# Kernel tuning notes

Hardware: AMD Instinct MI355X
Metric: run time of the kernel (lower is better)

Reference implementation:

```python
import jax, jax.numpy as jnp
from jax import lax
import numpy as np

B, D, P = 4096, 256, 512  # batch, encoded_space_dim (=d_prototypes), n_prototypes
BN_EPS = 1e-5  # torch BatchNorm eval with running_mean=0, running_var=1


def _conv(x, w, stride, pad):
    # x: NCHW, w: OIHW
    return lax.conv_general_dilated(x, w, (stride, stride), [(pad, pad), (pad, pad)],
                                    dimension_numbers=('NCHW', 'OIHW', 'NCHW'))


def _conv_t(x, w, stride, pad, out_pad):
    # torch ConvTranspose2d; w in torch layout [Cin, Cout, kh, kw]
    k = w.shape[2]
    wf = jnp.flip(w, (2, 3)).transpose(1, 0, 2, 3)  # -> OIHW, flipped
    lo = k - 1 - pad
    hi = k - 1 - pad + out_pad
    return lax.conv_general_dilated(x, wf, (1, 1), [(lo, hi), (lo, hi)],
                                    lhs_dilation=(stride, stride),
                                    dimension_numbers=('NCHW', 'OIHW', 'NCHW'))


def _bn(x, g, b):
    # eval-mode BatchNorm2d with running_mean=0, running_var=1
    s = g / jnp.sqrt(1.0 + BN_EPS)
    return x * s[None, :, None, None] + b[None, :, None, None]


def _bias(x, b):
    return x + b[None, :, None, None]


def setup_inputs() -> dict:
    key = jax.random.key(0)
    ks = jax.random.split(key, 32)
    n = jax.random.normal
    inp = {
        'x': jax.random.uniform(ks[0], (B, 1, 28, 28), jnp.float32),
        # encoder
        'w1': n(ks[1], (8, 1, 3, 3), jnp.float32) * 0.1, 'b1': jnp.zeros((8,), jnp.float32),
        'w2': n(ks[2], (16, 8, 3, 3), jnp.float32) * 0.1, 'b2': jnp.zeros((16,), jnp.float32),
        'g2': jnp.ones((16,), jnp.float32), 'bt2': jnp.zeros((16,), jnp.float32),
        'w3': n(ks[3], (D, 16, 3, 3), jnp.float32) * 0.1, 'b3': jnp.zeros((D,), jnp.float32),
        # prototypes (torch.rand init)
        'protolayer': jax.random.uniform(ks[4], (P, D, 1, 1), jnp.float32),
        # up layer (ConvTranspose2d(D, D, 5), torch layout [Cin,Cout,kh,kw])
        'wup': n(ks[5], (D, D, 5, 5), jnp.float32) * 0.02, 'bup': jnp.zeros((D,), jnp.float32),
        'gup': jnp.ones((D,), jnp.float32), 'btup': jnp.zeros((D,), jnp.float32),
        # decoder
        'wd1': n(ks[6], (D, 16, 3, 3), jnp.float32) * 0.05, 'bd1': jnp.zeros((16,), jnp.float32),
        'gd1': jnp.ones((16,), jnp.float32), 'btd1': jnp.zeros((16,), jnp.float32),
        'wd2': n(ks[7], (16, 8, 3, 3), jnp.float32) * 0.1, 'bd2': jnp.zeros((8,), jnp.float32),
        'gd2': jnp.ones((8,), jnp.float32), 'btd2': jnp.zeros((8,), jnp.float32),
        'wd3': n(ks[8], (8, 1, 3, 3), jnp.float32) * 0.1, 'bd3': jnp.zeros((1,), jnp.float32),
    }
    return inp


def reference(x, w1, b1, w2, b2, g2, bt2, w3, b3, protolayer,
              wup, bup, gup, btup,
              wd1, bd1, gd1, btd1, wd2, bd2, gd2, btd2, wd3, bd3):
    # ---- encoder: 28 -> 14 -> 7 -> 5 ----
    h = jax.nn.relu(_bias(_conv(x, w1, 2, 1), b1))
    h = jax.nn.relu(_bn(_bias(_conv(h, w2, 2, 1), b2), g2, bt2))
    h = jax.nn.relu(_bias(_conv(h, w3, 1, 0), b3))  # [B, D, 5, 5]

    # ---- l2 'convolution' with 1x1 prototypes ----
    p = protolayer[:, :, 0, 0]                                  # [P, D]
    x2_patch_sum = jnp.sum(h * h, axis=1)                       # ones-conv, 1x1 kernel -> channel sum [B,5,5]
    xp = jnp.einsum('bdhw,pd->bphw', h, p)                      # [B, P, 5, 5]
    p2 = jnp.sum(p * p, axis=1)                                 # [P]
    distances = jax.nn.relu(x2_patch_sum[:, None] - 2.0 * xp + p2[None, :, None, None])

    # min-pool over full spatial extent
    min_distances = jnp.min(distances, axis=(2, 3))             # [B, P]
    prototype_activations = -min_distances                      # 'linear' distance_2_similarity
    w = jax.nn.softmax(prototype_activations, axis=1)
    z = jnp.einsum('bp,pdkl->bdkl', w, protolayer)              # [B, D, 1, 1]

    # ---- up layer: 1 -> 5 ----
    z = jax.nn.relu(_bn(_bias(_conv_t(z, wup, 1, 0, 0), bup), gup, btup))

    # ---- decoder: 5 -> 7 -> 14 -> 28 ----
    h = jax.nn.relu(_bn(_bias(_conv_t(z, wd1, 1, 0, 0), bd1), gd1, btd1))
    h = jax.nn.relu(_bn(_bias(_conv_t(h, wd2, 2, 1, 1), bd2), gd2, btd2))
    out = jax.nn.sigmoid(_bias(_conv_t(h, wd3, 2, 1, 1), bd3))  # [B, 1, 28, 28]
    return out, min_distances
```

## Files before the change

kernel.cpp:

```cpp
#include <hip/hip_runtime.h>
#include <hip/hip_bf16.h>
#include <math.h>

#define NB 4096
#define DC 256
#define PC 512

typedef unsigned short ushort_t;
typedef __attribute__((ext_vector_type(4))) unsigned short us4;
typedef __attribute__((ext_vector_type(8))) unsigned short us8;
typedef __attribute__((ext_vector_type(8))) short s8v;
typedef __attribute__((ext_vector_type(4))) float f32x4;

__device__ __forceinline__ float bf16_to_f(ushort_t u) {
    union { unsigned int i; float f; } c;
    c.i = ((unsigned int)u) << 16;
    return c.f;
}
__device__ __forceinline__ ushort_t f2bf(float f) {
    union { float f; unsigned int u; } c; c.f = f;
    unsigned int r = c.u + 0x7fffu + ((c.u >> 16) & 1u);
    return (ushort_t)(r >> 16);
}

__global__ __launch_bounds__(256) void k_pre(
    const float* __restrict__ proto, float* __restrict__ p2,
    ushort_t* __restrict__ pfragHi, ushort_t* __restrict__ pfragLo,
    const float* __restrict__ w3, ushort_t* __restrict__ w3fH, ushort_t* __restrict__ w3fL,
    const float* __restrict__ w2, ushort_t* __restrict__ w2fH, ushort_t* __restrict__ w2fL,
    const float* __restrict__ wd1, ushort_t* __restrict__ wd1frag,
    const float* __restrict__ wup, ushort_t* __restrict__ wupfH, ushort_t* __restrict__ wupfL)
{
    int b = blockIdx.x, tid = threadIdx.x;
    __shared__ float red[256];
    if (b < 512) {
        int p = b, d = tid;
        float v = proto[p * DC + d];
        red[d] = v * v;
        __syncthreads();
        for (int s = 128; s > 0; s >>= 1) {
            if (d < s) red[d] += red[d + s];
            __syncthreads();
        }
        if (d == 0) p2[p] = red[0];
    } else if (b < 1024) {
        int idx = (b - 512) * 256 + tid;
        int j = idx & 7, l = (idx >> 3) & 63;
        int k0 = (idx >> 9) & 7, nt = idx >> 12;
        int n = nt * 16 + (l & 15);
        int k = k0 * 32 + (l >> 4) * 8 + j;
        float v = proto[n * DC + k];
        ushort_t hi = f2bf(v);
        pfragHi[idx] = hi;
        pfragLo[idx] = f2bf(v - bf16_to_f(hi));
    } else if (b < 1184) {
        int idx = (b - 1024) * 256 + tid;
        int j = idx & 7, l = (idx >> 3) & 63;
        int q = idx >> 9;
        int k0 = q % 5, nt = q / 5;
        int d = nt * 16 + (l & 15);
        int k = k0 * 32 + (l >> 4) * 8 + j;
        float v = (k < 144) ? w3[d * 144 + k] : 0.f;
        ushort_t hi = f2bf(v);
        w3fH[idx] = hi;
        w3fL[idx] = f2bf(v - bf16_to_f(hi));
    } else if (b < 1190) {
        int idx = (b - 1184) * 256 + tid;
        int j = idx & 7, l = (idx >> 3) & 63;
        int k0 = idx >> 9;
        int ch = l & 15;
        int k = k0 * 32 + (l >> 4) * 8 + j;
        float v = (k < 72) ? w2[ch * 72 + k] : 0.f;
        ushort_t hi = f2bf(v);
        w2fH[idx] = hi;
        w2fL[idx] = f2bf(v - bf16_to_f(hi));
    } else if (b < 1334) {
        int idx = (b - 1190) * 256 + tid;
        int j = idx & 7, l = (idx >> 3) & 63;
        int k0 = (idx >> 9) & 7, nt = idx >> 12;
        int n = nt * 16 + (l & 15);
        int k = k0 * 32 + (l >> 4) * 8 + j;
        wd1frag[idx] = f2bf(wd1[k * 144 + n]);
    } else {
        int idx = (b - 1334) * 256 + tid;
        int j = idx & 7, l = (idx >> 3) & 63;
        int k0 = (idx >> 9) & 7, nt = idx >> 12;
        int np = nt * 16 + (l & 15);
        int d = k0 * 32 + (l >> 4) * 8 + j;
        int pos = np >> 8, ch = np & 255;
        float v = wup[d * 6400 + ch * 25 + pos];
        ushort_t hi = f2bf(v);
        wupfH[idx] = hi;
        wupfL[idx] = f2bf(v - bf16_to_f(hi));
    }
}

__global__ __launch_bounds__(256) void k_pw2(
    const ushort_t* __restrict__ pfragHi, const ushort_t* __restrict__ pfragLo,
    const ushort_t* __restrict__ wupfH, const ushort_t* __restrict__ wupfL,
    ushort_t* __restrict__ PWfrag)
{
    int t = threadIdx.x;
    int w = t >> 6, l = t & 63, lr = l & 15, lg = l >> 4;
    int my = blockIdx.y;
    int ntb = blockIdx.x * 16 + w * 4;
    const s8v* AH = (const s8v*)pfragHi;
    const s8v* AL = (const s8v*)pfragLo;
    const s8v* BH = (const s8v*)wupfH;
    const s8v* BL = (const s8v*)wupfL;
    f32x4 acc[4];
#pragma unroll
    for (int q = 0; q < 4; q++) acc[q] = (f32x4){0.f, 0.f, 0.f, 0.f};
#pragma unroll
    for (int k0 = 0; k0 < 8; k0++) {
        s8v ah = AH[(my * 8 + k0) * 64 + l];
        s8v al = AL[(my * 8 + k0) * 64 + l];
#pragma unroll
        for (int q = 0; q < 4; q++) {
            s8v bh = BH[(size_t)((ntb + q) * 8 + k0) * 64 + l];
            s8v bl = BL[(size_t)((ntb + q) * 8 + k0) * 64 + l];
            acc[q] = __builtin_amdgcn_mfma_f32_16x16x32_bf16(ah, bh, acc[q], 0, 0, 0);
            acc[q] = __builtin_amdgcn_mfma_f32_16x16x32_bf16(al, bh, acc[q], 0, 0, 0);
            acc[q] = __builtin_amdgcn_mfma_f32_16x16x32_bf16(ah, bl, acc[q], 0, 0, 0);
        }
    }
#pragma unroll
    for (int q = 0; q < 4; q++) {
        int nt = ntb + q;
#pragma unroll
        for (int r = 0; r < 4; r++) {
            int p = my * 16 + lg * 4 + r;
            int k0p = p >> 5;
            int ll = ((p >> 3) & 3) * 16 + lr;
            int jj = p & 7;
            PWfrag[(((size_t)(nt * 16 + k0p) * 64) + ll) * 8 + jj] = f2bf(acc[q][r]);
        }
    }
}

__global__ __launch_bounds__(1024) void k_enc1(
    const float* __restrict__ x,
    const float* __restrict__ w1, const float* __restrict__ b1,
    const ushort_t* __restrict__ w2fH, const ushort_t* __restrict__ w2fL,
    const float* __restrict__ b2,
    const float* __restrict__ g2, const float* __restrict__ bt2,
    const ushort_t* __restrict__ w3fH, const ushort_t* __restrict__ w3fL,
    const float* __restrict__ b3,
    ushort_t* __restrict__ h3g)
{
    int b0 = blockIdx.x * 2;
    int t = threadIdx.x;
    int w = t >> 6, l = t & 63, lr = l & 15, lg = l >> 4;
    int tim = t >> 9, tt = t & 511;

    __shared__ __align__(16) unsigned char buf[51712];
    unsigned char* bufI = buf + tim * 25856;
    float* xb = (float*)bufI;
    float* h1 = (float*)(bufI + 3136);
    ushort_t* im2Hi = (ushort_t*)(bufI + 9408);
    float* h2 = (float*)(bufI + 22720);
    ushort_t* imHi = (ushort_t*)bufI;

    const float bnr = rsqrtf(1.0f + 1e-5f);

    const float* xg = x + (size_t)(b0 + tim) * 784;
    for (int i = tt; i < 784; i += 512) xb[i] = xg[i];
    for (int i = tt; i < 832; i += 512)
        ((float4*)(bufI + 9408))[i] = (float4){0.f, 0.f, 0.f, 0.f};
    __syncthreads();

    for (int o = tt; o < 1568; o += 512) {
        int c = o / 196, r = o % 196, y = r / 14, xc = r % 14;
        float acc = b1[c];
        for (int sy = 0; sy < 3; sy++) {
            int iy = 2 * y - 1 + sy;
            if ((unsigned)iy >= 28u) continue;
            for (int sx = 0; sx < 3; sx++) {
                int ix = 2 * xc - 1 + sx;
                if ((unsigned)ix >= 28u) continue;
                acc += w1[c * 9 + sy * 3 + sx] * xb[iy * 28 + ix];
            }
        }
        float v = fmaxf(acc, 0.f);
        ushort_t hi = f2bf(v);
        int kb = c * 9;
        int yA, syA, xA, sxA, yB = 0, xB = 0;
        bool hasYB, hasXB;
        if (y & 1) { yA = y >> 1; syA = 2; yB = yA + 1; hasYB = (yB < 7); }
        else       { yA = y >> 1; syA = 1; hasYB = false; }
        if (xc & 1) { xA = xc >> 1; sxA = 2; xB = xA + 1; hasXB = (xB < 7); }
        else        { xA = xc >> 1; sxA = 1; hasXB = false; }
        im2Hi[(yA * 7 + xA) * 104 + kb + syA * 3 + sxA] = hi;
        if (hasXB) im2Hi[(yA * 7 + xB) * 104 + kb + syA * 3] = hi;
        if (hasYB) {
            im2Hi[(yB * 7 + xA) * 104 + kb + sxA] = hi;
            if (hasXB) im2Hi[(yB * 7 + xB) * 104 + kb] = hi;
        }
    }
    __syncthreads();

    if ((w & 7) < 4) {
        int w4 = w & 3;
        f32x4 cc = {0, 0, 0, 0};
        const s8v* WH = (const s8v*)w2fH;
        const s8v* WL = (const s8v*)w2fL;
#pragma unroll
        for (int k0 = 0; k0 < 3; k0++) {
            s8v a0 = *(const s8v*)&im2Hi[(w4 * 16 + lr) * 104 + k0 * 32 + lg * 8];
            s8v bh = WH[k0 * 64 + l];
            s8v bl = WL[k0 * 64 + l];
            cc = __builtin_amdgcn_mfma_f32_16x16x32_bf16(a0, bh, cc, 0, 0, 0);
            cc = __builtin_amdgcn_mfma_f32_16x16x32_bf16(a0, bl, cc, 0, 0, 0);
        }
        int ch = lr;
        float s = g2[ch] * bnr, bb = b2[ch], bt = bt2[ch];
#pragma unroll
        for (int r = 0; r < 4; r++) {
            int pos = w4 * 16 + lg * 4 + r;
            if (pos < 49)
                h2[ch * 49 + pos] = fmaxf((cc[r] + bb) * s + bt, 0.f);
        }
    }
    __syncthreads();

    if (tt < 64) imHi[3600 + tt] = 0;
    for (int o = tt; o < 784; o += 512) {
        float v = h2[o];
        int ci = o / 49, rr = o % 49, iy = rr / 7, ixp = rr % 7;
        ushort_t hi = f2bf(v);
        int kb = ci * 9;
#pragma unroll
        for (int sy = 0; sy < 3; sy++) {
            int py = iy - sy;
            if ((unsigned)py < 5u) {
#pragma unroll
                for (int sx = 0; sx < 3; sx++) {
                    int px = ixp - sx;
                    if ((unsigned)px < 5u)
                        imHi[(py * 5 + px) * 144 + kb + sy * 3 + sx] = hi;
                }
            }
        }
    }
    __syncthreads();

    {
        const ushort_t* imHi0 = (const ushort_t*)buf;
        const ushort_t* imHi1 = (const ushort_t*)(buf + 25856);
        int nt = w;
        f32x4 c[2][2];
#pragma unroll
        for (int im = 0; im < 2; im++)
#pragma unroll
            for (int mt = 0; mt < 2; mt++) c[im][mt] = (f32x4){0.f, 0.f, 0.f, 0.f};
        const s8v* WH = (const s8v*)w3fH;
        const s8v* WL = (const s8v*)w3fL;
#pragma unroll
        for (int k0 = 0; k0 < 5; k0++) {
            s8v a00 = *(const s8v*)&imHi0[lr * 144 + k0 * 32 + lg * 8];
            s8v a01 = *(const s8v*)&imHi0[(16 + lr) * 144 + k0 * 32 + lg * 8];
            s8v a10 = *(const s8v*)&imHi1[lr * 144 + k0 * 32 + lg * 8];
            s8v a11 = *(const s8v*)&imHi1[(16 + lr) * 144 + k0 * 32 + lg * 8];
            s8v bh = WH[(nt * 5 + k0) * 64 + l];
            s8v bl = WL[(nt * 5 + k0) * 64 + l];
            c[0][0] = __builtin_amdgcn_mfma_f32_16x16x32_bf16(a00, bh, c[0][0], 0, 0, 0);
            c[0][1] = __builtin_amdgcn_mfma_f32_16x16x32_bf16(a01, bh, c[0][1], 0, 0, 0);
            c[0][0] = __builtin_amdgcn_mfma_f32_16x16x32_bf16(a00, bl, c[0][0], 0, 0, 0);
            c[0][1] = __builtin_amdgcn_mfma_f32_16x16x32_bf16(a01, bl, c[0][1], 0, 0, 0);
            c[1][0] = __builtin_amdgcn_mfma_f32_16x16x32_bf16(a10, bh, c[1][0], 0, 0, 0);
            c[1][1] = __builtin_amdgcn_mfma_f32_16x16x32_bf16(a11, bh, c[1][1], 0, 0, 0);
            c[1][0] = __builtin_amdgcn_mfma_f32_16x16x32_bf16(a10, bl, c[1][0], 0, 0, 0);
            c[1][1] = __builtin_amdgcn_mfma_f32_16x16x32_bf16(a11, bl, c[1][1], 0, 0, 0);
        }
        __syncthreads();
        int d = nt * 16 + lr;
        float bb = b3[d];
#pragma unroll
        for (int im = 0; im < 2; im++) {
            ushort_t* hs = (ushort_t*)(buf + im * 25856);
#pragma unroll
            for (int mt = 0; mt < 2; mt++) {
                f32x4 cv = c[im][mt];
#pragma unroll
                for (int r = 0; r < 4; r++) {
                    int pos = mt * 16 + lg * 4 + r;
                    if (pos < 25) {
                        float h = fmaxf(cv[r] + bb, 0.f);
                        hs[pos * 256 + d] = f2bf(h);
                    }
                }
            }
        }
    }
    __syncthreads();

    for (int i = t; i < 1600; i += 1024) {
        int im = i >= 800 ? 1 : 0;
        int idx = im ? i - 800 : i;
        *(us8*)&h3g[(size_t)(b0 + im) * 6400 + idx * 8] =
            *(const us8*)((const ushort_t*)(buf + im * 25856) + idx * 8);
    }
}

__global__ __launch_bounds__(1024) void k_enc2(
    const ushort_t* __restrict__ h3g,
    const ushort_t* __restrict__ pfragHi,
    const float* __restrict__ p2,
    float* __restrict__ md_out,
    ushort_t* __restrict__ Wsm)
{
    int t = threadIdx.x;
    int b0 = blockIdx.x * 2;
    int w = t >> 6, l = t & 63, lr = l & 15, lg = l >> 4;

    __shared__ __align__(16) ushort_t h3s[2][32][264];
    __shared__ float mds[2][512];
    __shared__ float x2sh[2][32];
    __shared__ float x2part[2][25][8];
    __shared__ float wred[2][16];

    for (int i = t; i < 2048; i += 1024) {
        int im = i >> 10, pos = (i >> 5) & 31, c8 = i & 31;
        us8 v = {0, 0, 0, 0, 0, 0, 0, 0};
        if (pos < 25)
            v = *(const us8*)&h3g[(size_t)(b0 + im) * 6400 + pos * 256 + c8 * 8];
        *(us8*)&h3s[im][pos][c8 * 8] = v;
    }
    __syncthreads();

    if (t < 400) {
        int im = t / 200, rest = t % 200;
        int pos = rest >> 3, ch = rest & 7;
        const ushort_t* hp = &h3s[im][pos][ch * 32];
        float s = 0.f;
#pragma unroll
        for (int i = 0; i < 32; i++) {
            float f = bf16_to_f(hp[i]);
            s = fmaf(f, f, s);
        }
        x2part[im][pos][ch] = s;
    }
    __syncthreads();
    if (t < 64) {
        int im = t >> 5, pos = t & 31;
        float s = 1e30f;
        if (pos < 25) {
            s = 0.f;
#pragma unroll
            for (int c = 0; c < 8; c++) s += x2part[im][pos][c];
        }
        x2sh[im][pos] = s;
    }
    __syncthreads();

    {
        f32x4 acc[2][2][2];
#pragma unroll
        for (int i = 0; i < 2; i++)
#pragma unroll
            for (int jm = 0; jm < 2; jm++)
#pragma unroll
                for (int mt = 0; mt < 2; mt++) acc[i][jm][mt] = (f32x4){0.f, 0.f, 0.f, 0.f};
        const s8v* BH = (const s8v*)pfragHi;
        s8v bhc[2], bhn[2];
#pragma unroll
        for (int ntq = 0; ntq < 2; ntq++) {
            int nt = w * 2 + ntq;
            bhc[ntq] = BH[(nt * 8 + 0) * 64 + l];
        }
        for (int k0 = 0; k0 < 8; k0++) {
            if (k0 < 7) {
#pragma unroll
                for (int ntq = 0; ntq < 2; ntq++) {
                    int nt = w * 2 + ntq;
                    bhn[ntq] = BH[(nt * 8 + k0 + 1) * 64 + l];
                }
            }
            s8v ah[2][2];
            ah[0][0] = *(const s8v*)&h3s[0][lr][k0 * 32 + lg * 8];
            ah[0][1] = *(const s8v*)&h3s[0][16 + lr][k0 * 32 + lg * 8];
            ah[1][0] = *(const s8v*)&h3s[1][lr][k0 * 32 + lg * 8];
            ah[1][1] = *(const s8v*)&h3s[1][16 + lr][k0 * 32 + lg * 8];
#pragma unroll
            for (int ntq = 0; ntq < 2; ntq++) {
                s8v bh = bhc[ntq];
#pragma unroll
                for (int im = 0; im < 2; im++) {
                    acc[ntq][im][0] = __builtin_amdgcn_mfma_f32_16x16x32_bf16(ah[im][0], bh, acc[ntq][im][0], 0, 0, 0);
                    acc[ntq][im][1] = __builtin_amdgcn_mfma_f32_16x16x32_bf16(ah[im][1], bh, acc[ntq][im][1], 0, 0, 0);
                }
            }
#pragma unroll
            for (int ntq = 0; ntq < 2; ntq++) bhc[ntq] = bhn[ntq];
        }
        float x2r[2][8];
#pragma unroll
        for (int im = 0; im < 2; im++)
#pragma unroll
            for (int r = 0; r < 4; r++) {
                x2r[im][r]     = x2sh[im][lg * 4 + r];
                x2r[im][4 + r] = x2sh[im][16 + lg * 4 + r];
            }
#pragma unroll
        for (int ntq = 0; ntq < 2; ntq++) {
            int pcol = (w * 2 + ntq) * 16 + lr;
            float p2v = p2[pcol];
#pragma unroll
            for (int im = 0; im < 2; im++) {
                float mm = 1e30f;
#pragma unroll
                for (int r = 0; r < 4; r++) {
                    float d0 = fmaxf(x2r[im][r]     - 2.f * acc[ntq][im][0][r] + p2v, 0.f);
                    float d1 = fmaxf(x2r[im][4 + r] - 2.f * acc[ntq][im][1][r] + p2v, 0.f);
                    mm = fminf(mm, fminf(d0, d1));
                }
                mm = fminf(mm, __shfl_xor(mm, 16));
                mm = fminf(mm, __shfl_xor(mm, 32));
                if (lg == 0) mds[im][pcol] = mm;
            }
        }
    }
    __syncthreads();

    int img = t >> 9, tt = t & 511;
    float mind = mds[img][tt];
    md_out[(size_t)(b0 + img) * PC + tt] = mind;
    float a = -mind;
    float mx = a;
#pragma unroll
    for (int off = 1; off < 64; off <<= 1) mx = fmaxf(mx, __shfl_xor(mx, off));
    int wv = w & 7;
    if (l == 0) wred[img][wv] = mx;
    __syncthreads();
    float m = wred[img][0];
#pragma unroll
    for (int i = 1; i < 8; i++) m = fmaxf(m, wred[img][i]);
    float e = expf(a - m);
    float sm = e;
#pragma unroll
    for (int off = 1; off < 64; off <<= 1) sm += __shfl_xor(sm, off);
    if (l == 0) wred[img][8 + wv] = sm;
    __syncthreads();
    float ssum = wred[img][8];
#pragma unroll
    for (int i = 9; i < 16; i++) ssum += wred[img][i];
    Wsm[(size_t)(b0 + img) * PC + tt] = f2bf(e / ssum);
}

__global__ __launch_bounds__(512) void k_zup2(
    const ushort_t* __restrict__ Wsm,
    const ushort_t* __restrict__ PWfrag,
    const float* __restrict__ bup, const float* __restrict__ gup,
    const float* __restrict__ btup,
    ushort_t* __restrict__ zupT)
{
    __shared__ __align__(16) ushort_t Bsh[2][8192];
    int t = threadIdx.x;
    int w = t >> 6, l = t & 63;
    int n0 = blockIdx.x * 128;
    int m0 = blockIdx.y * 128;
    int row = m0 + w * 16 + (l & 15);
    int krow = (l >> 4) * 8;
    f32x4 acc[8];
#pragma unroll
    for (int i = 0; i < 8; i++) acc[i] = (f32x4){0.f, 0.f, 0.f, 0.f};
    const s8v* B = (const s8v*)PWfrag;
    int base = blockIdx.x * 8 * 16;

    {
        s8v v0 = B[(size_t)(base + (t >> 6) * 16 + 0) * 64 + (t & 63)];
        s8v v1 = B[(size_t)(base + (t >> 6) * 16 + 1) * 64 + (t & 63)];
        *(s8v*)&Bsh[0][t * 8] = v0;
        *(s8v*)&Bsh[0][4096 + t * 8] = v1;
    }
    __syncthreads();
    for (int r = 0; r < 8; r++) {
        int cur = r & 1;
        if (r < 7) {
            s8v v0 = B[(size_t)(base + (t >> 6) * 16 + 2 * r + 2) * 64 + (t & 63)];
            s8v v1 = B[(size_t)(base + (t >> 6) * 16 + 2 * r + 3) * 64 + (t & 63)];
            *(s8v*)&Bsh[cur ^ 1][t * 8] = v0;
            *(s8v*)&Bsh[cur ^ 1][4096 + t * 8] = v1;
        }
#pragma unroll
        for (int kk = 0; kk < 2; kk++) {
            int k0 = 2 * r + kk;
            s8v a = *(const s8v*)&Wsm[(size_t)row * 512 + k0 * 32 + krow];
#pragma unroll
            for (int nt = 0; nt < 8; nt++) {
                s8v bb = *(const s8v*)&Bsh[cur][kk * 4096 + (nt * 64 + l) * 8];
                acc[nt] = __builtin_amdgcn_mfma_f32_16x16x32_bf16(a, bb, acc[nt], 0, 0, 0);
            }
        }
        __syncthreads();
    }

    const float bnr = rsqrtf(1.0f + 1e-5f);
    int rowbase = m0 + w * 16 + (l >> 4) * 4;
#pragma unroll
    for (int nt = 0; nt < 8; nt++) {
        int n = n0 + nt * 16 + (l & 15);
        int ch = n & 255;
        float sc = gup[ch] * bnr, bb = bup[ch], bt = btup[ch];
#pragma unroll
        for (int r = 0; r < 4; r++) {
            float v = (acc[nt][r] + bb) * sc + bt;
            zupT[(size_t)(rowbase + r) * 6400 + n] = f2bf(fmaxf(v, 0.f));
        }
    }
}

template<int CLS, int NCO>
__device__ __forceinline__ void wd2_piece(
    const float* hb, float* hout, const float* w2sT,
    const float* bd2, const float* gd2, const float* btd2,
    float bnr, int r, int c, int co0)
{
    const int cy = CLS >> 1, cx = CLS & 1;
    float acc[NCO];
#pragma unroll
    for (int q = 0; q < NCO; q++) acc[q] = 0.f;
#pragma unroll
    for (int ty = 0; ty < 1 + cy; ty++) {
        int iy = r + ty;
        int sy = cy ? (ty ? 0 : 2) : 1;
#pragma unroll
        for (int tx = 0; tx < 1 + cx; tx++) {
            int ix = c + tx;
            int sx = cx ? (tx ? 0 : 2) : 1;
            const float* wp = &w2sT[(sy * 3 + sx) * 128];
            int hoff = iy * 8 + ix;
            float h[16];
#pragma unroll
            for (int ci = 0; ci < 16; ci++) h[ci] = hb[ci * 64 + hoff];
#pragma unroll
            for (int q = 0; q < NCO; q++) {
                const float* wc = &wp[(co0 + q) * 16];
                float a = acc[q];
#pragma unroll
                for (int ci = 0; ci < 16; ci++) a = fmaf(h[ci], wc[ci], a);
                acc[q] = a;
            }
        }
    }
    int y = 2 * r + cy, x = 2 * c + cx;
#pragma unroll
    for (int q = 0; q < NCO; q++) {
        int co = co0 + q;
        float v = (acc[q] + bd2[co]) * (gd2[co] * bnr) + btd2[co];
        hout[co * 225 + y * 15 + x] = fmaxf(v, 0.f);
    }
}

template<int CLS, int NROW>
__device__ __forceinline__ void wd3_piece(
    const float* h2b, const float* w3sT, float bd30,
    float* og, int l, int row0)
{
    const int cy = CLS >> 1, cx = CLS & 1;
    const int NIT = (NROW * 16 + 63) / 64;
#pragma unroll
    for (int j = 0; j < NIT; j++) {
        int idx = l + 64 * j;
        int row = idx >> 4, col = idx & 15;
        if (row < NROW && col < 14) {
            int rr = row0 + row;
            float a = bd30;
#pragma unroll
            for (int ty = 0; ty < 1 + cy; ty++) {
                int iy = rr + ty;
                int sy = cy ? (ty ? 0 : 2) : 1;
#pragma unroll
                for (int tx = 0; tx < 1 + cx; tx++) {
                    int ix = col + tx;
                    int sx = cx ? (tx ? 0 : 2) : 1;
                    const float* wp = &w3sT[(sy * 3 + sx) * 8];
                    int hoff = iy * 15 + ix;
#pragma unroll
                    for (int ci = 0; ci < 8; ci++)
                        a = fmaf(h2b[ci * 225 + hoff], wp[ci], a);
                }
            }
            int y = 2 * rr + cy, x = 2 * col + cx;
            og[y * 28 + x] = 1.f / (1.f + expf(-a));
        }
    }
}

__global__ __launch_bounds__(512) void k_dtail(
    const ushort_t* __restrict__ zupT,
    const ushort_t* __restrict__ wd1frag,
    const float* __restrict__ bd1, const float* __restrict__ gd1, const float* __restrict__ btd1,
    const float* __restrict__ wd2, const float* __restrict__ bd2,
    const float* __restrict__ gd2, const float* __restrict__ btd2,
    const float* __restrict__ wd3, const float* __restrict__ bd3,
    float* __restrict__ out0)
{
    int b0 = blockIdx.x * 2, t = threadIdx.x;
    int w = t >> 6, l = t & 63, lr = l & 15, lg = l >> 4;
    int g = w >> 2, wv = w & 3, tg = t & 255;
    __shared__ __align__(16) unsigned char dbuf[33792];
    __shared__ float hd1p[2][16][64];
    __shared__ float w2sT[9 * 8 * 16];
    __shared__ float w3sT[9 * 8];
    ushort_t* zAb = (ushort_t*)dbuf;
    float* Psb = (float*)dbuf;

    const float bnr = rsqrtf(1.0f + 1e-5f);

    for (int c = t; c < 1600; c += 512) {
        int im = c / 800, cc = c % 800;
        *(us8*)&zAb[im * 8448 + (cc >> 5) * 264 + (cc & 31) * 8] =
            *(const us8*)&zupT[(size_t)(b0 + im) * 6400 + cc * 8];
    }
    for (int i = t; i < 2048; i += 512) ((float*)hd1p)[i] = 0.f;
    for (int i = t; i < 1152; i += 512) {
        int s = i >> 7, rest = i & 127;
        int co = rest >> 4, ci = rest & 15;
        w2sT[i] = wd2[(ci * 8 + co) * 9 + s];
    }
    if (t < 72) {
        int s = t >> 3, ci = t & 7;
        w3sT[t] = wd3[ci * 9 + s];
    }
    __syncthreads();

    {
        f32x4 acc[3][2];
#pragma unroll
        for (int i = 0; i < 3; i++)
#pragma unroll
            for (int mt = 0; mt < 2; mt++) acc[i][mt] = (f32x4){0.f, 0.f, 0.f, 0.f};
        const s8v* B = (const s8v*)wd1frag;
        for (int k0 = 0; k0 < 8; k0++) {
            s8v a0 = *(const s8v*)&zAb[g * 8448 + lr * 264 + k0 * 32 + lg * 8];
            s8v a1 = *(const s8v*)&zAb[g * 8448 + (16 + lr) * 264 + k0 * 32 + lg * 8];
#pragma unroll
            for (int i = 0; i < 3; i++) {
                int nt = wv + 4 * i;
                if (nt < 9) {
                    s8v bb = B[(nt * 8 + k0) * 64 + l];
                    acc[i][0] = __builtin_amdgcn_mfma_f32_16x16x32_bf16(a0, bb, acc[i][0], 0, 0, 0);
                    acc[i][1] = __builtin_amdgcn_mfma_f32_16x16x32_bf16(a1, bb, acc[i][1], 0, 0, 0);
                }
            }
        }
        __syncthreads();
#pragma unroll
        for (int i = 0; i < 3; i++) {
            int nt = wv + 4 * i;
            if (nt < 9) {
                int col = nt * 16 + lr;
#pragma unroll
                for (int mt = 0; mt < 2; mt++)
#pragma unroll
                    for (int r = 0; r < 4; r++) {
                        int pos = mt * 16 + lg * 4 + r;
                        if (pos < 25) Psb[g * 3700 + pos * 148 + col] = acc[i][mt][r];
                    }
            }
        }
    }
    __syncthreads();

    for (int o = tg; o < 784; o += 256) {
        int co = o / 49, rr = o % 49, y = rr / 7, xx = rr % 7;
        float a = bd1[co];
        int sy0 = y - 4 > 0 ? y - 4 : 0, sy1 = y < 2 ? y : 2;
        for (int sy = sy0; sy <= sy1; sy++) {
            int iy = y - sy;
            int sx0 = xx - 4 > 0 ? xx - 4 : 0, sx1 = xx < 2 ? xx : 2;
            for (int sx = sx0; sx <= sx1; sx++) {
                int ix = xx - sx;
                a += Psb[g * 3700 + (iy * 5 + ix) * 148 + co * 9 + sy * 3 + sx];
            }
        }
        float v = a * (gd1[co] * bnr) + btd1[co];
        hd1p[g][co][y * 8 + xx] = fmaxf(v, 0.f);
    }
    __syncthreads();

    {
        if (t < 464) {
            int im = t / 232, rest = t % 232;
            int co = rest / 29, s = rest % 29;
            int yy = (s < 15) ? 14 : (s - 15);
            int xx2 = (s < 15) ? s : 14;
            ((float*)dbuf)[im * 1808 + co * 225 + yy * 15 + xx2] = 0.f;
        }
        if (l < 56 && (l & 7) < 7) {
            int r = l >> 3, c = l & 7;
            const float* hb = &hd1p[g][0][0];
            float* hout = (float*)dbuf + g * 1808;
            if (wv == 0) {
                wd2_piece<3, 4>(hb, hout, w2sT, bd2, gd2, btd2, bnr, r, c, 0);
                wd2_piece<0, 2>(hb, hout, w2sT, bd2, gd2, btd2, bnr, r, c, 0);
            } else if (wv == 1) {
                wd2_piece<3, 4>(hb, hout, w2sT, bd2, gd2, btd2, bnr, r, c, 4);
                wd2_piece<0, 2>(hb, hout, w2sT, bd2, gd2, btd2, bnr, r, c, 2);
            } else if (wv == 2) {
                wd2_piece<1, 8>(hb, hout, w2sT, bd2, gd2, btd2, bnr, r, c, 0);
                wd2_piece<0, 2>(hb, hout, w2sT, bd2, gd2, btd2, bnr, r, c, 4);
            } else {
                wd2_piece<2, 8>(hb, hout, w2sT, bd2, gd2, btd2, bnr, r, c, 0);
                wd2_piece<0, 2>(hb, hout, w2sT, bd2, gd2, btd2, bnr, r, c, 6);
            }
        }
    }
    __syncthreads();

    {
        const float* h2b = (const float*)dbuf + g * 1808;
        float* og = out0 + (size_t)(b0 + g) * 784;
        float bd30 = bd3[0];
        if (wv == 0) {
            wd3_piece<3, 7>(h2b, w3sT, bd30, og, l, 0);
            wd3_piece<0, 7>(h2b, w3sT, bd30, og, l, 0);
        } else if (wv == 1) {
            wd3_piece<3, 7>(h2b, w3sT, bd30, og, l, 7);
            wd3_piece<0, 7>(h2b, w3sT, bd30, og, l, 7);
        } else if (wv == 2) {
            wd3_piece<1, 14>(h2b, w3sT, bd30, og, l, 0);
        } else {
            wd3_piece<2, 14>(h2b, w3sT, bd30, og, l, 0);
        }
    }
}

extern "C" void kernel_launch(void* const* d_in, const int* in_sizes, int n_in,
                              void* d_out, int out_size, void* d_ws, size_t ws_size,
                              hipStream_t stream) {
    const float* x    = (const float*)d_in[0];
    const float* w1   = (const float*)d_in[1];
    const float* b1   = (const float*)d_in[2];
    const float* w2   = (const float*)d_in[3];
    const float* b2   = (const float*)d_in[4];
    const float* g2   = (const float*)d_in[5];
    const float* bt2  = (const float*)d_in[6];
    const float* w3   = (const float*)d_in[7];
    const float* b3   = (const float*)d_in[8];
    const float* proto= (const float*)d_in[9];
    const float* wup  = (const float*)d_in[10];
    const float* bup  = (const float*)d_in[11];
    const float* gup  = (const float*)d_in[12];
    const float* btup = (const float*)d_in[13];
    const float* wd1  = (const float*)d_in[14];
    const float* bd1  = (const float*)d_in[15];
    const float* gd1  = (const float*)d_in[16];
    const float* btd1 = (const float*)d_in[17];
    const float* wd2  = (const float*)d_in[18];
    const float* bd2  = (const float*)d_in[19];
    const float* gd2  = (const float*)d_in[20];
    const float* btd2 = (const float*)d_in[21];
    const float* wd3  = (const float*)d_in[22];
    const float* bd3  = (const float*)d_in[23];

    float* out0   = (float*)d_out;
    float* out_md = out0 + (size_t)NB * 784;

    float*    p2      = (float*)d_ws;
    float*    pad0    = p2 + 512;
    ushort_t* pfragHi = (ushort_t*)(pad0 + 131072);
    ushort_t* pfragLo = pfragHi + 131072;
    ushort_t* w3fH    = pfragLo + 131072;
    ushort_t* w3fL    = w3fH + 40960;
    ushort_t* w2fH    = w3fL + 40960;
    ushort_t* w2fL    = w2fH + 1536;
    ushort_t* wd1frag = w2fL + 1536;
    ushort_t* wupfH   = wd1frag + 36864;
    ushort_t* wupfL   = wupfH + 1638400;
    ushort_t* PWfrag  = wupfL + 1638400;
    ushort_t* Wsm     = PWfrag + 3276800;
    ushort_t* BIG     = Wsm + 2097152;
    ushort_t* h3g     = BIG;
    ushort_t* zupT    = BIG;

    hipLaunchKernelGGL(k_pre, dim3(7734), dim3(256), 0, stream,
                       proto, p2, pfragHi, pfragLo, w3, w3fH, w3fL,
                       w2, w2fH, w2fL, wd1, wd1frag, wup, wupfH, wupfL);
    hipLaunchKernelGGL(k_pw2, dim3(25, 32), dim3(256), 0, stream,
                       pfragHi, pfragLo, wupfH, wupfL, PWfrag);
    hipLaunchKernelGGL(k_enc1, dim3(NB / 2), dim3(1024), 0, stream,
                       x, w1, b1, w2fH, w2fL, b2, g2, bt2, w3fH, w3fL, b3, h3g);
    hipLaunchKernelGGL(k_enc2, dim3(NB / 2), dim3(1024), 0, stream,
                       h3g, pfragHi, p2, out_md, Wsm);
    hipLaunchKernelGGL(k_zup2, dim3(50, 32), dim3(512), 0, stream,
                       Wsm, PWfrag, bup, gup, btup, zupT);
    hipLaunchKernelGGL(k_dtail, dim3(NB / 2), dim3(512), 0, stream,
                       zupT, wd1frag, bd1, gd1, btd1, wd2, bd2, gd2, btd2, wd3, bd3, out0);
}
```

Before: 237.3 us.

## Double k_dtail block to 1024 threads with eight waves per image

The decoder tail kernel now runs 1024 threads per block, so each of the two images gets eight waves instead of four. The MFMA n-tiles, the wd1 reduction loop, and the wd2 and wd3 transposed-conv pieces are redistributed so each wave does about half as much work. The goal is to cut the per-block serial latency of the small decoder stages. The cost is more idle waves, since the 9 n-tiles leave wave slots unused and the uneven pieces leave some waves with less work, plus higher register pressure under the larger launch bound.

```diff
diff --git a/kernel.cpp b/kernel.cpp
--- a/kernel.cpp
+++ b/kernel.cpp
@@ -587,7 +587,7 @@
     }
 }
 
-__global__ __launch_bounds__(512) void k_dtail(
+__global__ __launch_bounds__(1024) void k_dtail(
     const ushort_t* __restrict__ zupT,
     const ushort_t* __restrict__ wd1frag,
     const float* __restrict__ bd1, const float* __restrict__ gd1, const float* __restrict__ btd1,
@@ -598,7 +598,7 @@
 {
     int b0 = blockIdx.x * 2, t = threadIdx.x;
     int w = t >> 6, l = t & 63, lr = l & 15, lg = l >> 4;
-    int g = w >> 2, wv = w & 3, tg = t & 255;
+    int g = w >> 3, wv = w & 7;
     __shared__ __align__(16) unsigned char dbuf[33792];
     __shared__ float hd1p[2][16][64];
     __shared__ float w2sT[9 * 8 * 16];
@@ -608,13 +608,13 @@
 
     const float bnr = rsqrtf(1.0f + 1e-5f);
 
-    for (int c = t; c < 1600; c += 512) {
+    for (int c = t; c < 1600; c += 1024) {
         int im = c / 800, cc = c % 800;
         *(us8*)&zAb[im * 8448 + (cc >> 5) * 264 + (cc & 31) * 8] =
             *(const us8*)&zupT[(size_t)(b0 + im) * 6400 + cc * 8];
     }
-    for (int i = t; i < 2048; i += 512) ((float*)hd1p)[i] = 0.f;
-    for (int i = t; i < 1152; i += 512) {
+    for (int i = t; i < 2048; i += 1024) ((float*)hd1p)[i] = 0.f;
+    for (int i = t; i < 1152; i += 1024) {
         int s = i >> 7, rest = i & 127;
         int co = rest >> 4, ci = rest & 15;
         w2sT[i] = wd2[(ci * 8 + co) * 9 + s];
@@ -626,9 +626,9 @@
     __syncthreads();
 
     {
-        f32x4 acc[3][2];
-#pragma unroll
-        for (int i = 0; i < 3; i++)
+        f32x4 acc[2][2];
+#pragma unroll
+        for (int i = 0; i < 2; i++)
 #pragma unroll
             for (int mt = 0; mt < 2; mt++) acc[i][mt] = (f32x4){0.f, 0.f, 0.f, 0.f};
         const s8v* B = (const s8v*)wd1frag;
@@ -636,8 +636,8 @@
             s8v a0 = *(const s8v*)&zAb[g * 8448 + lr * 264 + k0 * 32 + lg * 8];
             s8v a1 = *(const s8v*)&zAb[g * 8448 + (16 + lr) * 264 + k0 * 32 + lg * 8];
 #pragma unroll
-            for (int i = 0; i < 3; i++) {
-                int nt = wv + 4 * i;
+            for (int i = 0; i < 2; i++) {
+                int nt = wv + 8 * i;
                 if (nt < 9) {
                     s8v bb = B[(nt * 8 + k0) * 64 + l];
                     acc[i][0] = __builtin_amdgcn_mfma_f32_16x16x32_bf16(a0, bb, acc[i][0], 0, 0, 0);
@@ -647,8 +647,8 @@
         }
         __syncthreads();
 #pragma unroll
-        for (int i = 0; i < 3; i++) {
-            int nt = wv + 4 * i;
+        for (int i = 0; i < 2; i++) {
+            int nt = wv + 8 * i;
             if (nt < 9) {
                 int col = nt * 16 + lr;
 #pragma unroll
@@ -663,20 +663,23 @@
     }
     __syncthreads();
 
-    for (int o = tg; o < 784; o += 256) {
-        int co = o / 49, rr = o % 49, y = rr / 7, xx = rr % 7;
-        float a = bd1[co];
-        int sy0 = y - 4 > 0 ? y - 4 : 0, sy1 = y < 2 ? y : 2;
-        for (int sy = sy0; sy <= sy1; sy++) {
-            int iy = y - sy;
-            int sx0 = xx - 4 > 0 ? xx - 4 : 0, sx1 = xx < 2 ? xx : 2;
-            for (int sx = sx0; sx <= sx1; sx++) {
-                int ix = xx - sx;
-                a += Psb[g * 3700 + (iy * 5 + ix) * 148 + co * 9 + sy * 3 + sx];
-            }
-        }
-        float v = a * (gd1[co] * bnr) + btd1[co];
-        hd1p[g][co][y * 8 + xx] = fmaxf(v, 0.f);
+    {
+        int tg = t & 511;
+        for (int o = tg; o < 784; o += 512) {
+            int co = o / 49, rr = o % 49, y = rr / 7, xx = rr % 7;
+            float a = bd1[co];
+            int sy0 = y - 4 > 0 ? y - 4 : 0, sy1 = y < 2 ? y : 2;
+            for (int sy = sy0; sy <= sy1; sy++) {
+                int iy = y - sy;
+                int sx0 = xx - 4 > 0 ? xx - 4 : 0, sx1 = xx < 2 ? xx : 2;
+                for (int sx = sx0; sx <= sx1; sx++) {
+                    int ix = xx - sx;
+                    a += Psb[g * 3700 + (iy * 5 + ix) * 148 + co * 9 + sy * 3 + sx];
+                }
+            }
+            float v = a * (gd1[co] * bnr) + btd1[co];
+            hd1p[g][co][y * 8 + xx] = fmaxf(v, 0.f);
+        }
     }
     __syncthreads();
 
@@ -692,18 +695,19 @@
             int r = l >> 3, c = l & 7;
             const float* hb = &hd1p[g][0][0];
             float* hout = (float*)dbuf + g * 1808;
-            if (wv == 0) {
-                wd2_piece<3, 4>(hb, hout, w2sT, bd2, gd2, btd2, bnr, r, c, 0);
-                wd2_piece<0, 2>(hb, hout, w2sT, bd2, gd2, btd2, bnr, r, c, 0);
-            } else if (wv == 1) {
-                wd2_piece<3, 4>(hb, hout, w2sT, bd2, gd2, btd2, bnr, r, c, 4);
-                wd2_piece<0, 2>(hb, hout, w2sT, bd2, gd2, btd2, bnr, r, c, 2);
-            } else if (wv == 2) {
-                wd2_piece<1, 8>(hb, hout, w2sT, bd2, gd2, btd2, bnr, r, c, 0);
-                wd2_piece<0, 2>(hb, hout, w2sT, bd2, gd2, btd2, bnr, r, c, 4);
-            } else {
-                wd2_piece<2, 8>(hb, hout, w2sT, bd2, gd2, btd2, bnr, r, c, 0);
-                wd2_piece<0, 2>(hb, hout, w2sT, bd2, gd2, btd2, bnr, r, c, 6);
+            switch (wv) {
+                case 0: wd2_piece<3, 2>(hb, hout, w2sT, bd2, gd2, btd2, bnr, r, c, 0);
+                        wd2_piece<0, 2>(hb, hout, w2sT, bd2, gd2, btd2, bnr, r, c, 0); break;
+                case 1: wd2_piece<3, 2>(hb, hout, w2sT, bd2, gd2, btd2, bnr, r, c, 2);
+                        wd2_piece<0, 2>(hb, hout, w2sT, bd2, gd2, btd2, bnr, r, c, 2); break;
+                case 2: wd2_piece<3, 2>(hb, hout, w2sT, bd2, gd2, btd2, bnr, r, c, 4);
+                        wd2_piece<0, 2>(hb, hout, w2sT, bd2, gd2, btd2, bnr, r, c, 4); break;
+                case 3: wd2_piece<3, 2>(hb, hout, w2sT, bd2, gd2, btd2, bnr, r, c, 6);
+                        wd2_piece<0, 2>(hb, hout, w2sT, bd2, gd2, btd2, bnr, r, c, 6); break;
+                case 4: wd2_piece<1, 4>(hb, hout, w2sT, bd2, gd2, btd2, bnr, r, c, 0); break;
+                case 5: wd2_piece<1, 4>(hb, hout, w2sT, bd2, gd2, btd2, bnr, r, c, 4); break;
+                case 6: wd2_piece<2, 4>(hb, hout, w2sT, bd2, gd2, btd2, bnr, r, c, 0); break;
+                default: wd2_piece<2, 4>(hb, hout, w2sT, bd2, gd2, btd2, bnr, r, c, 4); break;
             }
         }
     }
@@ -713,16 +717,17 @@
         const float* h2b = (const float*)dbuf + g * 1808;
         float* og = out0 + (size_t)(b0 + g) * 784;
         float bd30 = bd3[0];
-        if (wv == 0) {
-            wd3_piece<3, 7>(h2b, w3sT, bd30, og, l, 0);
-            wd3_piece<0, 7>(h2b, w3sT, bd30, og, l, 0);
-        } else if (wv == 1) {
-            wd3_piece<3, 7>(h2b, w3sT, bd30, og, l, 7);
-            wd3_piece<0, 7>(h2b, w3sT, bd30, og, l, 7);
-        } else if (wv == 2) {
-            wd3_piece<1, 14>(h2b, w3sT, bd30, og, l, 0);
-        } else {
-            wd3_piece<2, 14>(h2b, w3sT, bd30, og, l, 0);
+        switch (wv) {
+            case 0: wd3_piece<3, 4>(h2b, w3sT, bd30, og, l, 0); break;
+            case 1: wd3_piece<3, 4>(h2b, w3sT, bd30, og, l, 4); break;
+            case 2: wd3_piece<3, 4>(h2b, w3sT, bd30, og, l, 8); break;
+            case 3: wd3_piece<3, 2>(h2b, w3sT, bd30, og, l, 12); break;
+            case 4: wd3_piece<1, 7>(h2b, w3sT, bd30, og, l, 0);
+                    wd3_piece<0, 7>(h2b, w3sT, bd30, og, l, 0); break;
+            case 5: wd3_piece<1, 7>(h2b, w3sT, bd30, og, l, 7);
+                    wd3_piece<0, 7>(h2b, w3sT, bd30, og, l, 7); break;
+            case 6: wd3_piece<2, 7>(h2b, w3sT, bd30, og, l, 0); break;
+            default: wd3_piece<2, 7>(h2b, w3sT, bd30, og, l, 7); break;
         }
     }
 }
@@ -786,6 +791,6 @@
                        h3g, pfragHi, p2, out_md, Wsm);
     hipLaunchKernelGGL(k_zup2, dim3(50, 32), dim3(512), 0, stream,
                        Wsm, PWfrag, bup, gup, btup, zupT);
-    hipLaunchKernelGGL(k_dtail, dim3(NB / 2), dim3(512), 0, stream,
+    hipLaunchKernelGGL(k_dtail, dim3(NB / 2), dim3(1024), 0, stream,
                        zupT, wd1frag, bd1, gd1, btd1, wd2, bd2, gd2, btd2, wd3, bd3, out0);
 }
```

New measurement: 257.1 us. +8.3%, slower.
